# Optimization experiments

Measured on AMD Instinct MI355X. Metric: run time of the kernel, lower is better.

Reference implementation:

```python
import jax, jax.numpy as jnp
import numpy as np

TAU = 0.5
EPS = 1e-08


def setup_inputs() -> dict:
    key = jax.random.key(0)
    k1, k2 = jax.random.split(key)
    B, D = 8192, 128
    z_a = jax.random.normal(k1, (B, D), dtype=jnp.float32)
    z_b = jax.random.normal(k2, (B, D), dtype=jnp.float32)
    return {"z_a": z_a, "z_b": z_b}


def reference(z_a, z_b):
    B = z_a.shape[0]
    N = 2 * B
    z = jnp.concatenate([z_a, z_b], axis=0)           # [2B, D]
    sim = (z @ z.T) / TAU                             # [2B, 2B]
    sp = jax.nn.softplus(sim)
    # zero out self-similarity (diagonal)
    idx = jnp.arange(N)
    sp = sp.at[idx, idx].set(0.0)
    denom = jnp.maximum(sp.sum(axis=-1), EPS)         # [2B]
    pos_idx = (idx + B) % N
    sp_pos = sp[idx, pos_idx]                         # [2B]
    log_p = jnp.log(jnp.maximum(sp_pos, EPS)) - jnp.log(denom)
    return -log_p.mean()
```

## Files before the change

### kernel.cpp

```cpp
#include <hip/hip_runtime.h>
#include <hip/hip_bf16.h>

constexpr int Bh = 8192;
constexpr int Nn = 16384;
constexpr int Dd = 128;
constexpr float EPS = 1e-8f;
constexpr float LN2 = 0.69314718056f;

constexpr int K_TILES = 8;
constexpr int N_TILES = 8256;
constexpr int N_BLOCKS = N_TILES / K_TILES;

typedef short bf16x8 __attribute__((ext_vector_type(8)));
typedef float f32x4 __attribute__((ext_vector_type(4)));

__global__ __launch_bounds__(256) void convert_kernel(const float4* __restrict__ za,
                                                      const float4* __restrict__ zb,
                                                      ushort* __restrict__ z,
                                                      float* __restrict__ rowsum,
                                                      float* __restrict__ out) {
    const int t = blockIdx.x * 256 + threadIdx.x;
    constexpr int Q = (Bh * Dd) / 4;
    const float SCL = 1.69864363f;
    float4 v = (t < Q) ? za[t] : zb[t - Q];
    union { ushort4 u4; __hip_bfloat16 h[4]; } cv;
    cv.h[0] = __float2bfloat16(v.x * SCL);
    cv.h[1] = __float2bfloat16(v.y * SCL);
    cv.h[2] = __float2bfloat16(v.z * SCL);
    cv.h[3] = __float2bfloat16(v.w * SCL);
    ((ushort4*)z)[t] = cv.u4;
    if (t < Nn) rowsum[t] = 0.f;
    if (t == 0) out[0] = 0.f;
}

__device__ __forceinline__ int row_tile_of(int g) {
    int t = (int)((257.0f - sqrtf(66049.0f - 8.0f * (float)g)) * 0.5f);
    t = t < 0 ? 0 : (t > 127 ? 127 : t);
    while (t * (257 - t) / 2 > g) --t;
    while ((t + 1) * (256 - t) / 2 <= g) ++t;
    return t;
}

__device__ __forceinline__ void flush_rs(float* __restrict__ rowsum, int rowW,
                                         float (&rs)[2][4], int q, int c) {
#pragma unroll
    for (int s = 0; s < 2; ++s)
#pragma unroll
        for (int r = 0; r < 4; ++r) {
            float v = rs[s][r];
            v += __shfl_xor(v, 1);
            v += __shfl_xor(v, 2);
            v += __shfl_xor(v, 4);
            v += __shfl_xor(v, 8);
            if (c == 0) atomicAdd(&rowsum[rowW + s * 16 + q * 4 + r], v);
            rs[s][r] = 0.f;
        }
}

__device__ __forceinline__ void colflush(float* __restrict__ rowsum,
                                         float (&csumP)[8], int C0P, int lane, int c) {
#pragma unroll
    for (int st = 0; st < 8; ++st) {
        float v = csumP[st];
        v += __shfl_xor(v, 16);
        v += __shfl_xor(v, 32);
        if (lane < 16) atomicAdd(&rowsum[C0P + st * 16 + c], v);
    }
}

__device__ __forceinline__ void stage_tile(const ushort* __restrict__ z, ushort* lbuf,
                                           int C0, int wave, int lane) {
#pragma unroll
    for (int i = 0; i < 8; ++i) {
        const int chunk = wave * 8 + i;
        const int r = (chunk << 2) + (lane >> 4);
        const int bl = ((lane & 15) ^ (r & 15)) << 4;
        const char* gp = (const char*)z + (((size_t)(C0 + r)) << 8) + bl;
        ushort* lp = lbuf + (chunk << 9);
        __builtin_amdgcn_global_load_lds((const __attribute__((address_space(1))) void*)gp,
                                         (__attribute__((address_space(3))) void*)lp,
                                         16, 0, 0);
    }
}

__global__ __launch_bounds__(256) void main_kernel(const ushort* __restrict__ z,
                                                   float* __restrict__ rowsum,
                                                   float* __restrict__ pospair) {
    __shared__ ushort ldsb[2][16384];

    const int tid = threadIdx.x;
    const int wave = tid >> 6;
    const int lane = tid & 63;
    const int q = lane >> 4;
    const int c = lane & 15;
    const int g0 = blockIdx.x * K_TILES;

    int tr = row_tile_of(g0);
    int ct = tr + (g0 - tr * (257 - tr) / 2);

    int O[4];
#pragma unroll
    for (int kt = 0; kt < 4; ++kt) O[kt] = (c << 8) + ((((q + 4 * kt) ^ c)) << 4);

    bf16x8 afrag[2][4];
    float rs[2][4];
#pragma unroll
    for (int s = 0; s < 2; ++s)
#pragma unroll
        for (int r = 0; r < 4; ++r) rs[s][r] = 0.f;

    float csumP[8];
    int C0P = 0;
    bool pendP = false;
    int cur_tr = -1, rowW = 0, cur = 0;

    stage_tile(z, &ldsb[0][0], ct << 7, wave, lane);
    __syncthreads();

    for (int j = 0; j < K_TILES; ++j) {
        const int C0 = ct << 7;
        const bool diag = (ct == tr);

        if (tr != cur_tr) {
            if (cur_tr >= 0) flush_rs(rowsum, rowW, rs, q, c);
            cur_tr = tr;
            rowW = (tr << 7) + wave * 32;
#pragma unroll
            for (int s = 0; s < 2; ++s) {
                const ushort* ap = z + (size_t)(rowW + s * 16 + c) * Dd;
#pragma unroll
                for (int kt = 0; kt < 4; ++kt)
                    afrag[s][kt] = *(const bf16x8*)(ap + kt * 32 + q * 8);
            }
        }

        if (pendP) { colflush(rowsum, csumP, C0P, lane, c); pendP = false; }

        int trN = tr, ctN = ct + 1;
        if (ctN == 128) { trN = tr + 1; ctN = trN; }
        if (j + 1 < K_TILES) stage_tile(z, &ldsb[cur ^ 1][0], ctN << 7, wave, lane);

        const char* lb = (const char*)&ldsb[cur][0];
        float csum[8];
#pragma unroll
        for (int st = 0; st < 8; ++st) csum[st] = 0.f;

#pragma unroll
        for (int st = 0; st < 8; ++st) {
            bf16x8 bcur[4];
#pragma unroll
            for (int kt = 0; kt < 4; ++kt)
                bcur[kt] = *(const bf16x8*)(lb + O[kt] + st * 4096);

            f32x4 acc[2] = {{0.f,0.f,0.f,0.f},{0.f,0.f,0.f,0.f}};
#pragma unroll
            for (int kt = 0; kt < 4; ++kt) {
#pragma unroll
                for (int s = 0; s < 2; ++s)
                    acc[s] = __builtin_amdgcn_mfma_f32_16x16x32_bf16(afrag[s][kt], bcur[kt], acc[s], 0, 0, 0);
            }
            const int gc0 = C0 + st * 16;
#pragma unroll
            for (int s = 0; s < 2; ++s) {
                const int R = rowW + s * 16;
                float sp[4];
#pragma unroll
                for (int r = 0; r < 4; ++r) {
                    float u = acc[s][r];
                    float e = __builtin_amdgcn_exp2f(-fabsf(u));
                    sp[r] = fmaxf(u, 0.f) + __builtin_amdgcn_logf(1.f + e);
                }
                if (diag && gc0 == R) {
#pragma unroll
                    for (int r = 0; r < 4; ++r)
                        if (c == q * 4 + r) sp[r] = 0.f;
                }
                if (gc0 == (R ^ Bh)) {
#pragma unroll
                    for (int r = 0; r < 4; ++r)
                        if (c == q * 4 + r) pospair[R + q * 4 + r] = sp[r];
                }
#pragma unroll
                for (int r = 0; r < 4; ++r) rs[s][r] += sp[r];
                if (!diag) csum[st] += (sp[0] + sp[1]) + (sp[2] + sp[3]);
            }
        }

        if (!diag) {
#pragma unroll
            for (int st = 0; st < 8; ++st) csumP[st] = csum[st];
            C0P = C0;
            pendP = true;
        }

        __syncthreads();
        cur ^= 1;
        tr = trN;
        ct = ctN;
    }

    if (pendP) colflush(rowsum, csumP, C0P, lane, c);
    if (cur_tr >= 0) flush_rs(rowsum, rowW, rs, q, c);
}

__global__ __launch_bounds__(1024) void finalize_kernel(const float* __restrict__ rowsum,
                                                        const float* __restrict__ pospair,
                                                        float* __restrict__ out) {
    __shared__ float red[16];
    const int i = blockIdx.x * 1024 + threadIdx.x;
    float denom = fmaxf(LN2 * rowsum[i], EPS);
    float sp = fmaxf(LN2 * pospair[i & (Bh - 1)], EPS);
    float acc = __logf(sp) - __logf(denom);
#pragma unroll
    for (int m = 1; m < 64; m <<= 1) acc += __shfl_xor(acc, m);
    if ((threadIdx.x & 63) == 0) red[threadIdx.x >> 6] = acc;
    __syncthreads();
    if (threadIdx.x < 16) {
        float v = red[threadIdx.x];
        v += __shfl_xor(v, 1);
        v += __shfl_xor(v, 2);
        v += __shfl_xor(v, 4);
        v += __shfl_xor(v, 8);
        if (threadIdx.x == 0) atomicAdd(out, -v / (float)Nn);
    }
}

extern "C" void kernel_launch(void* const* d_in, const int* in_sizes, int n_in,
                              void* d_out, int out_size, void* d_ws, size_t ws_size,
                              hipStream_t stream) {
    const float* za = (const float*)d_in[0];
    const float* zb = (const float*)d_in[1];

    ushort* z = (ushort*)d_ws;
    float* rowsum = (float*)((char*)d_ws + (size_t)Nn * Dd * 2);
    float* pospair = rowsum + Nn;
    float* out = (float*)d_out;

    convert_kernel<<<2048, 256, 0, stream>>>((const float4*)za, (const float4*)zb, z, rowsum, out);
    main_kernel<<<N_BLOCKS, 256, 0, stream>>>(z, rowsum, pospair);
    finalize_kernel<<<16, 1024, 0, stream>>>(rowsum, pospair, out);
}
```

Measured before the change: 177.2 us.

## Use 8 waves per block with 16 rows each and LDS column-sum buffer

Result: slower. 182.2 us (+2.8%).

```diff
diff --git a/kernel.cpp b/kernel.cpp
--- a/kernel.cpp
+++ b/kernel.cpp
@@ -42,37 +42,24 @@
 }
 
 __device__ __forceinline__ void flush_rs(float* __restrict__ rowsum, int rowW,
-                                         float (&rs)[2][4], int q, int c) {
-#pragma unroll
-    for (int s = 0; s < 2; ++s)
-#pragma unroll
-        for (int r = 0; r < 4; ++r) {
-            float v = rs[s][r];
-            v += __shfl_xor(v, 1);
-            v += __shfl_xor(v, 2);
-            v += __shfl_xor(v, 4);
-            v += __shfl_xor(v, 8);
-            if (c == 0) atomicAdd(&rowsum[rowW + s * 16 + q * 4 + r], v);
-            rs[s][r] = 0.f;
-        }
-}
-
-__device__ __forceinline__ void colflush(float* __restrict__ rowsum,
-                                         float (&csumP)[8], int C0P, int lane, int c) {
-#pragma unroll
-    for (int st = 0; st < 8; ++st) {
-        float v = csumP[st];
-        v += __shfl_xor(v, 16);
-        v += __shfl_xor(v, 32);
-        if (lane < 16) atomicAdd(&rowsum[C0P + st * 16 + c], v);
+                                         float (&rs)[4], int q, int c) {
+#pragma unroll
+    for (int r = 0; r < 4; ++r) {
+        float v = rs[r];
+        v += __shfl_xor(v, 1);
+        v += __shfl_xor(v, 2);
+        v += __shfl_xor(v, 4);
+        v += __shfl_xor(v, 8);
+        if (c == 0) atomicAdd(&rowsum[rowW + q * 4 + r], v);
+        rs[r] = 0.f;
     }
 }
 
 __device__ __forceinline__ void stage_tile(const ushort* __restrict__ z, ushort* lbuf,
                                            int C0, int wave, int lane) {
 #pragma unroll
-    for (int i = 0; i < 8; ++i) {
-        const int chunk = wave * 8 + i;
+    for (int i = 0; i < 4; ++i) {
+        const int chunk = wave * 4 + i;
         const int r = (chunk << 2) + (lane >> 4);
         const int bl = ((lane & 15) ^ (r & 15)) << 4;
         const char* gp = (const char*)z + (((size_t)(C0 + r)) << 8) + bl;
@@ -83,10 +70,11 @@
     }
 }
 
-__global__ __launch_bounds__(256) void main_kernel(const ushort* __restrict__ z,
+__global__ __launch_bounds__(512) void main_kernel(const ushort* __restrict__ z,
                                                    float* __restrict__ rowsum,
                                                    float* __restrict__ pospair) {
     __shared__ ushort ldsb[2][16384];
+    __shared__ float colbuf[2][128];
 
     const int tid = threadIdx.x;
     const int wave = tid >> 6;
@@ -98,52 +86,50 @@
     int tr = row_tile_of(g0);
     int ct = tr + (g0 - tr * (257 - tr) / 2);
 
+    if (tid < 256) colbuf[tid >> 7][tid & 127] = 0.f;
+
     int O[4];
 #pragma unroll
     for (int kt = 0; kt < 4; ++kt) O[kt] = (c << 8) + ((((q + 4 * kt) ^ c)) << 4);
 
-    bf16x8 afrag[2][4];
-    float rs[2][4];
-#pragma unroll
-    for (int s = 0; s < 2; ++s)
-#pragma unroll
-        for (int r = 0; r < 4; ++r) rs[s][r] = 0.f;
-
-    float csumP[8];
+    bf16x8 afrag[4];
+    float rs[4] = {0.f, 0.f, 0.f, 0.f};
+
     int C0P = 0;
-    bool pendP = false;
+    bool flushP = false;
     int cur_tr = -1, rowW = 0, cur = 0;
 
     stage_tile(z, &ldsb[0][0], ct << 7, wave, lane);
     __syncthreads();
 
     for (int j = 0; j < K_TILES; ++j) {
+        const int pcur = j & 1;
         const int C0 = ct << 7;
         const bool diag = (ct == tr);
 
         if (tr != cur_tr) {
             if (cur_tr >= 0) flush_rs(rowsum, rowW, rs, q, c);
             cur_tr = tr;
-            rowW = (tr << 7) + wave * 32;
-#pragma unroll
-            for (int s = 0; s < 2; ++s) {
-                const ushort* ap = z + (size_t)(rowW + s * 16 + c) * Dd;
-#pragma unroll
-                for (int kt = 0; kt < 4; ++kt)
-                    afrag[s][kt] = *(const bf16x8*)(ap + kt * 32 + q * 8);
-            }
+            rowW = (tr << 7) + wave * 16;
+            const ushort* ap = z + (size_t)(rowW + c) * Dd;
+#pragma unroll
+            for (int kt = 0; kt < 4; ++kt)
+                afrag[kt] = *(const bf16x8*)(ap + kt * 32 + q * 8);
         }
 
-        if (pendP) { colflush(rowsum, csumP, C0P, lane, c); pendP = false; }
+        if (flushP) {
+            if (tid < 128) {
+                atomicAdd(&rowsum[C0P + tid], colbuf[pcur ^ 1][tid]);
+                colbuf[pcur ^ 1][tid] = 0.f;
+            }
+            flushP = false;
+        }
 
         int trN = tr, ctN = ct + 1;
         if (ctN == 128) { trN = tr + 1; ctN = trN; }
         if (j + 1 < K_TILES) stage_tile(z, &ldsb[cur ^ 1][0], ctN << 7, wave, lane);
 
         const char* lb = (const char*)&ldsb[cur][0];
-        float csum[8];
-#pragma unroll
-        for (int st = 0; st < 8; ++st) csum[st] = 0.f;
 
 #pragma unroll
         for (int st = 0; st < 8; ++st) {
@@ -152,46 +138,41 @@
             for (int kt = 0; kt < 4; ++kt)
                 bcur[kt] = *(const bf16x8*)(lb + O[kt] + st * 4096);
 
-            f32x4 acc[2] = {{0.f,0.f,0.f,0.f},{0.f,0.f,0.f,0.f}};
-#pragma unroll
-            for (int kt = 0; kt < 4; ++kt) {
-#pragma unroll
-                for (int s = 0; s < 2; ++s)
-                    acc[s] = __builtin_amdgcn_mfma_f32_16x16x32_bf16(afrag[s][kt], bcur[kt], acc[s], 0, 0, 0);
-            }
+            f32x4 acc = {0.f, 0.f, 0.f, 0.f};
+#pragma unroll
+            for (int kt = 0; kt < 4; ++kt)
+                acc = __builtin_amdgcn_mfma_f32_16x16x32_bf16(afrag[kt], bcur[kt], acc, 0, 0, 0);
+
             const int gc0 = C0 + st * 16;
-#pragma unroll
-            for (int s = 0; s < 2; ++s) {
-                const int R = rowW + s * 16;
-                float sp[4];
-#pragma unroll
-                for (int r = 0; r < 4; ++r) {
-                    float u = acc[s][r];
-                    float e = __builtin_amdgcn_exp2f(-fabsf(u));
-                    sp[r] = fmaxf(u, 0.f) + __builtin_amdgcn_logf(1.f + e);
-                }
-                if (diag && gc0 == R) {
-#pragma unroll
-                    for (int r = 0; r < 4; ++r)
-                        if (c == q * 4 + r) sp[r] = 0.f;
-                }
-                if (gc0 == (R ^ Bh)) {
-#pragma unroll
-                    for (int r = 0; r < 4; ++r)
-                        if (c == q * 4 + r) pospair[R + q * 4 + r] = sp[r];
-                }
-#pragma unroll
-                for (int r = 0; r < 4; ++r) rs[s][r] += sp[r];
-                if (!diag) csum[st] += (sp[0] + sp[1]) + (sp[2] + sp[3]);
+            const int R = rowW;
+            float sp[4];
+#pragma unroll
+            for (int r = 0; r < 4; ++r) {
+                float u = acc[r];
+                float e = __builtin_amdgcn_exp2f(-fabsf(u));
+                sp[r] = fmaxf(u, 0.f) + __builtin_amdgcn_logf(1.f + e);
+            }
+            if (diag && gc0 == R) {
+#pragma unroll
+                for (int r = 0; r < 4; ++r)
+                    if (c == q * 4 + r) sp[r] = 0.f;
+            }
+            if (gc0 == (R ^ Bh)) {
+#pragma unroll
+                for (int r = 0; r < 4; ++r)
+                    if (c == q * 4 + r) pospair[R + q * 4 + r] = sp[r];
+            }
+#pragma unroll
+            for (int r = 0; r < 4; ++r) rs[r] += sp[r];
+            if (!diag) {
+                float v = (sp[0] + sp[1]) + (sp[2] + sp[3]);
+                v += __shfl_xor(v, 16);
+                v += __shfl_xor(v, 32);
+                if (lane < 16) atomicAdd(&colbuf[pcur][st * 16 + c], v);
             }
         }
 
-        if (!diag) {
-#pragma unroll
-            for (int st = 0; st < 8; ++st) csumP[st] = csum[st];
-            C0P = C0;
-            pendP = true;
-        }
+        if (!diag) { C0P = C0; flushP = true; }
 
         __syncthreads();
         cur ^= 1;
@@ -199,7 +180,8 @@
         ct = ctN;
     }
 
-    if (pendP) colflush(rowsum, csumP, C0P, lane, c);
+    if (flushP && tid < 128)
+        atomicAdd(&rowsum[C0P + tid], colbuf[(K_TILES - 1) & 1][tid]);
     if (cur_tr >= 0) flush_rs(rowsum, rowW, rs, q, c);
 }
 
@@ -237,6 +219,6 @@
     float* out = (float*)d_out;
 
     convert_kernel<<<2048, 256, 0, stream>>>((const float4*)za, (const float4*)zb, z, rowsum, out);
-    main_kernel<<<N_BLOCKS, 256, 0, stream>>>(z, rowsum, pospair);
+    main_kernel<<<N_BLOCKS, 512, 0, stream>>>(z, rowsum, pospair);
     finalize_kernel<<<16, 1024, 0, stream>>>(rowsum, pospair, out);
 }
```
